# Optimization experiments

Hardware: AMD Instinct MI355X
Metric: run time of the kernel (lower is better)

## Reference

```python
import jax, jax.numpy as jnp
import numpy as np


def setup_inputs() -> dict:
    key = jax.random.key(0)
    B, C, A, P, N = 4, 1, 180, 384, 256
    sinogram = jax.random.normal(key, (B, C, A, P), dtype=jnp.float32)
    # projection angles uniformly covering [0, pi)
    thetas = jnp.linspace(0.0, np.pi, A, endpoint=False).astype(jnp.float32)
    # uniformly spaced detector positions centered at 0, unit spacing
    positions = jnp.arange(P, dtype=jnp.float32) - (P - 1) / 2.0
    return {"sinogram": sinogram, "thetas": thetas, "positions": positions, "image_size": N}


def reference(sinogram, thetas, positions, image_size):
    """Radon backprojection: image[y,x] = sum_a interp(sinogram[a], x*cos+y*sin)."""
    B, C, A, P = sinogram.shape
    N = image_size
    # pixel-center coordinates, image centered at origin (y axis pointing up)
    c = jnp.arange(N, dtype=sinogram.dtype) - (N - 1) / 2.0
    xs = c[None, :]          # [1, N]
    ys = -c[:, None]         # [N, 1]
    cos = jnp.cos(thetas)[:, None, None]  # [A, 1, 1]
    sin = jnp.sin(thetas)[:, None, None]
    t = xs[None] * cos + ys[None] * sin   # [A, N, N] detector coordinate per (angle, pixel)
    # fractional index into the (uniform) detector position grid
    dp = positions[1] - positions[0]
    f = (t - positions[0]) / dp           # [A, N, N]
    i0 = jnp.floor(f)
    w = f - i0                            # linear interpolation weight
    valid = (i0 >= 0) & (i0 <= P - 2)     # rays falling inside the detector
    i0c = jnp.clip(i0, 0, P - 2).astype(jnp.int32)
    idx = i0c.reshape(A, N * N)[None, None]          # [1, 1, A, N*N]
    v0 = jnp.take_along_axis(sinogram, idx, axis=3)  # [B, C, A, N*N]
    v1 = jnp.take_along_axis(sinogram, idx + 1, axis=3)
    wf = w.reshape(A, N * N)[None, None]
    vm = valid.reshape(A, N * N)[None, None]
    val = jnp.where(vm, v0 * (1.0 - wf) + v1 * wf, 0.0)
    return val.sum(axis=2).reshape(B, C, N, N)
```

## Files before the change

### kernel.cpp

```cpp
#include <hip/hip_runtime.h>
#include <hip/hip_fp16.h>
#include <cmath>


#define ACHUNKS 4

typedef __fp16 half2v __attribute__((ext_vector_type(2)));

__device__ __forceinline__ half2v as_h2(unsigned u) {
    union { unsigned u; half2v h; } x; x.u = u; return x.h;
}

__global__ __launch_bounds__(256) void radon_pack_zero(
    const float* __restrict__ sino,
    const float* __restrict__ thetas,
    const float* __restrict__ positions,
    uint4* __restrict__ packed,
    float2* __restrict__ trig,
    float4* __restrict__ out4,
    int A, int P, int PES, int bstride, int nout4)
{
    const int gidx = blockIdx.x * 256 + threadIdx.x;
    if (gidx < nout4) out4[gidx] = make_float4(0.f, 0.f, 0.f, 0.f);

    const int a = gidx / PES;
    const int j = gidx - a * PES;
    if (a >= A) return;

    const float p0     = positions[0];
    const float inv_dp = 1.0f / (positions[1] - p0);
    if (j == 0) {
        float th = thetas[a];
        trig[a] = make_float2(cosf(th) * inv_dp, sinf(th) * inv_dp);
        if (a == 0) trig[A] = make_float2(-p0 * inv_dp, 0.0f);
    }

    uint4 e = make_uint4(0, 0, 0, 0);
    if (j >= 1 && j <= P - 1) {
        const float* s = sino + (size_t)a * P + (j - 1);
        unsigned* ep = (unsigned*)&e;
#pragma unroll
        for (int b = 0; b < 4; ++b) {
            float2 v = *(const float2*)(s + (size_t)b * bstride);
            half2v h = __builtin_amdgcn_cvt_pkrtz(v.x, v.y);
            union { half2v h; unsigned u; } cvt; cvt.h = h;
            ep[b] = cvt.u;
        }
    }
    packed[(size_t)a * PES + j] = e;
}

__global__ __launch_bounds__(256) void radon_gather_at(
    const uint4* __restrict__ packed,
    const float2* __restrict__ trig,
    float* __restrict__ out,
    int A, int P, int PES, int N, int chunk)
{
    const int tid = threadIdx.x;
    const int nn  = N * N;

    const int w  = tid >> 6;
    const int l  = tid & 63;
    const int lx = l & 15;
    const int ly = l >> 4;
    const int tilesx = N >> 6;
    const int bx = blockIdx.x % tilesx;
    const int by = blockIdx.x / tilesx;
    const int x  = (bx << 6) + (w << 4) + lx;
    const int y  = (by << 2) + ly;
    const int pix = y * N + x;

    const int a0  = blockIdx.y * chunk;
    const int a1  = min(A, a0 + chunk);

    const float half = (float)(N - 1) * 0.5f;
    const float cx = (float)x - half;
    const float cy = half - (float)y;
    const float q0 = trig[A].x;

    float acc0 = 0.f, acc1 = 0.f, acc2 = 0.f, acc3 = 0.f;

#pragma unroll 4
    for (int a = a0; a < a1; ++a) {
        float2 t  = trig[a];
        float f   = fmaf(cx, t.x, fmaf(cy, t.y, q0));
        float i0f = floorf(f);
        float w_  = f - i0f;
        int   i0  = (int)i0f;
        int   j   = min(max(i0, -1), P - 1) + 1;

        half2v w2 = __builtin_amdgcn_cvt_pkrtz(1.0f - w_, w_);
        uint4 e = packed[(size_t)a * PES + j];
        acc0 = __builtin_amdgcn_fdot2(as_h2(e.x), w2, acc0, false);
        acc1 = __builtin_amdgcn_fdot2(as_h2(e.y), w2, acc1, false);
        acc2 = __builtin_amdgcn_fdot2(as_h2(e.z), w2, acc2, false);
        acc3 = __builtin_amdgcn_fdot2(as_h2(e.w), w2, acc3, false);
    }

    float* op = out + pix;
    atomicAdd(op,                  acc0);
    atomicAdd(op + (size_t)nn,     acc1);
    atomicAdd(op + (size_t)2 * nn, acc2);
    atomicAdd(op + (size_t)3 * nn, acc3);
}

__global__ __launch_bounds__(256) void radon_direct_kernel(
    const float* __restrict__ sino,
    const float* __restrict__ thetas,
    const float* __restrict__ positions,
    float* __restrict__ out,
    int A, int P, int N, int BC)
{
    const int nn  = N * N;
    const int pix = blockIdx.x * blockDim.x + threadIdx.x;
    if (pix >= nn) return;
    const float p0     = positions[0];
    const float inv_dp = 1.0f / (positions[1] - p0);
    const int x = pix % N;
    const int y = pix / N;
    const float half = (float)(N - 1) * 0.5f;
    const float cx = (float)x - half;
    const float cy = half - (float)y;
    for (int b = 0; b < BC; ++b) {
        float acc = 0.0f;
        for (int a = 0; a < A; ++a) {
            float th = thetas[a];
            float f  = (cx * cosf(th) + cy * sinf(th) - p0) * inv_dp;
            float i0f = floorf(f);
            int i0 = (int)i0f;
            float w = f - i0f;
            float m = (i0 >= 0 && i0 <= P - 2) ? 1.0f : 0.0f;
            int ic = min(max(i0, 0), P - 2);
            const float* row = sino + ((size_t)b * A + a) * P + ic;
            acc = fmaf(m, fmaf(w, row[1] - row[0], row[0]), acc);
        }
        out[(size_t)b * nn + pix] = acc;
    }
}

extern "C" void kernel_launch(void* const* d_in, const int* in_sizes, int n_in,
                              void* d_out, int out_size, void* d_ws, size_t ws_size,
                              hipStream_t stream) {
    const float* sino      = (const float*)d_in[0];
    const float* thetas    = (const float*)d_in[1];
    const float* positions = (const float*)d_in[2];
    float* out             = (float*)d_out;

    const int A  = in_sizes[1];
    const int P  = in_sizes[2];
    const int BC = in_sizes[0] / (A * P);
    const int N  = (int)lroundf(sqrtf((float)(out_size / BC)));
    const int nn = N * N;
    const int bstride = A * P;

    const int PES   = (P + 2 + 63) & ~63;
    const int chunk = (A + ACHUNKS - 1) / ACHUNKS;
    const int nout4 = nn;

    const size_t packed_bytes = (size_t)A * PES * sizeof(uint4);
    const size_t trig_bytes   = (size_t)(A + 1) * sizeof(float2);
    const size_t need = packed_bytes + trig_bytes;

    const bool fast = (BC == 4) && (A <= 1024) && (P >= 2)
                   && (N % 64 == 0) && (ws_size >= need);

    if (fast) {
        uint4*  packed = (uint4*)d_ws;
        float2* trig   = (float2*)((char*)d_ws + packed_bytes);

        dim3 block(256);
        const unsigned gp = (unsigned)(((size_t)A * PES > (size_t)nout4
                                        ? (size_t)A * PES : (size_t)nout4) + 255) / 256;
        radon_pack_zero<<<dim3(gp), block, 0, stream>>>(
            sino, thetas, positions, packed, trig, (float4*)out,
            A, P, PES, bstride, nout4);

        dim3 gpart((N / 64) * (N / 4), ACHUNKS);
        radon_gather_at<<<gpart, block, 0, stream>>>(
            packed, trig, out, A, P, PES, N, chunk);
    } else {
        dim3 block(256);
        dim3 grid((nn + 255) / 256);
        radon_direct_kernel<<<grid, block, 0, stream>>>(
            sino, thetas, positions, out, A, P, N, BC);
    }
}
```

Before: 71.05 us.

## Replace global atomics with in-block LDS reduction across angle groups

The four angle chunks, previously spread over separate blocks that combined results with global atomicAdd, now run as four 256-thread groups inside one 1024-thread block. Each group writes its partial sums to shared memory, and after a barrier each thread sums one (batch, pixel) value and stores it directly. This removes the output zeroing pass in the pack kernel and all global atomics. In exchange the grid has four times fewer but larger blocks, which may reduce occupancy flexibility and load balance, and it adds 16KB of LDS per block.

Result: no change. 71.08 us (median of 2 runs) (+0.0%).

```diff
diff --git a/kernel.cpp b/kernel.cpp
--- a/kernel.cpp
+++ b/kernel.cpp
@@ -3,7 +3,7 @@
 #include <cmath>
 
 
-#define ACHUNKS 4
+#define AGROUPS 4
 
 typedef __fp16 half2v __attribute__((ext_vector_type(2)));
 
@@ -11,18 +11,15 @@
     union { unsigned u; half2v h; } x; x.u = u; return x.h;
 }
 
-__global__ __launch_bounds__(256) void radon_pack_zero(
+__global__ __launch_bounds__(256) void radon_pack(
     const float* __restrict__ sino,
     const float* __restrict__ thetas,
     const float* __restrict__ positions,
     uint4* __restrict__ packed,
     float2* __restrict__ trig,
-    float4* __restrict__ out4,
-    int A, int P, int PES, int bstride, int nout4)
+    int A, int P, int PES, int bstride)
 {
     const int gidx = blockIdx.x * 256 + threadIdx.x;
-    if (gidx < nout4) out4[gidx] = make_float4(0.f, 0.f, 0.f, 0.f);
-
     const int a = gidx / PES;
     const int j = gidx - a * PES;
     if (a >= A) return;
@@ -50,17 +47,21 @@
     packed[(size_t)a * PES + j] = e;
 }
 
-__global__ __launch_bounds__(256) void radon_gather_at(
+__global__ __launch_bounds__(1024) void radon_gather_red(
     const uint4* __restrict__ packed,
     const float2* __restrict__ trig,
     float* __restrict__ out,
     int A, int P, int PES, int N, int chunk)
 {
+    __shared__ float red[AGROUPS][256][4];
+
     const int tid = threadIdx.x;
     const int nn  = N * N;
+    const int g   = tid >> 8;
+    const int p   = tid & 255;
 
-    const int w  = tid >> 6;
-    const int l  = tid & 63;
+    const int w  = p >> 6;
+    const int l  = p & 63;
     const int lx = l & 15;
     const int ly = l >> 4;
     const int tilesx = N >> 6;
@@ -68,10 +69,9 @@
     const int by = blockIdx.x / tilesx;
     const int x  = (bx << 6) + (w << 4) + lx;
     const int y  = (by << 2) + ly;
-    const int pix = y * N + x;
 
-    const int a0  = blockIdx.y * chunk;
-    const int a1  = min(A, a0 + chunk);
+    const int a0 = g * chunk;
+    const int a1 = min(A, a0 + chunk);
 
     const float half = (float)(N - 1) * 0.5f;
     const float cx = (float)x - half;
@@ -97,11 +97,22 @@
         acc3 = __builtin_amdgcn_fdot2(as_h2(e.w), w2, acc3, false);
     }
 
-    float* op = out + pix;
-    atomicAdd(op,                  acc0);
-    atomicAdd(op + (size_t)nn,     acc1);
-    atomicAdd(op + (size_t)2 * nn, acc2);
-    atomicAdd(op + (size_t)3 * nn, acc3);
+    red[g][p][0] = acc0;
+    red[g][p][1] = acc1;
+    red[g][p][2] = acc2;
+    red[g][p][3] = acc3;
+    __syncthreads();
+
+    const int b2 = tid >> 8;
+    const int p2 = tid & 255;
+    float s = red[0][p2][b2] + red[1][p2][b2]
+            + red[2][p2][b2] + red[3][p2][b2];
+
+    const int w2_ = p2 >> 6;
+    const int l2  = p2 & 63;
+    const int x2  = (bx << 6) + (w2_ << 4) + (l2 & 15);
+    const int y2  = (by << 2) + (l2 >> 4);
+    out[(size_t)b2 * nn + y2 * N + x2] = s;
 }
 
 __global__ __launch_bounds__(256) void radon_direct_kernel(
@@ -154,8 +165,7 @@
     const int bstride = A * P;
 
     const int PES   = (P + 2 + 63) & ~63;
-    const int chunk = (A + ACHUNKS - 1) / ACHUNKS;
-    const int nout4 = nn;
+    const int chunk = (A + AGROUPS - 1) / AGROUPS;
 
     const size_t packed_bytes = (size_t)A * PES * sizeof(uint4);
     const size_t trig_bytes   = (size_t)(A + 1) * sizeof(float2);
@@ -169,14 +179,13 @@
         float2* trig   = (float2*)((char*)d_ws + packed_bytes);
 
         dim3 block(256);
-        const unsigned gp = (unsigned)(((size_t)A * PES > (size_t)nout4
-                                        ? (size_t)A * PES : (size_t)nout4) + 255) / 256;
-        radon_pack_zero<<<dim3(gp), block, 0, stream>>>(
-            sino, thetas, positions, packed, trig, (float4*)out,
-            A, P, PES, bstride, nout4);
+        dim3 gpack(((unsigned)(A * PES) + 255) / 256);
+        radon_pack<<<gpack, block, 0, stream>>>(
+            sino, thetas, positions, packed, trig, A, P, PES, bstride);
 
-        dim3 gpart((N / 64) * (N / 4), ACHUNKS);
-        radon_gather_at<<<gpart, block, 0, stream>>>(
+        dim3 gblock(1024);
+        dim3 ggat((N / 64) * (N / 4));
+        radon_gather_red<<<ggat, gblock, 0, stream>>>(
             packed, trig, out, A, P, PES, N, chunk);
     } else {
         dim3 block(256);
```
